# Kernel tuning notes

Hardware: AMD Instinct MI355X
Metric: run time of the kernel (lower is better)

The kernel has to match this reference:

```python
import jax, jax.numpy as jnp
import numpy as np

B, C, H, W = 8, 512, 64, 64
K = 19       # num classes (Cityscapes)
CT = 256     # transform channels


def _proj(x, w, g, b):
    # 1x1 conv (no bias) + folded eval-mode BatchNorm (per-channel scale g, bias b) + ReLU
    # x: [B,Cin,H,W], w: [Cout,Cin]
    y = jnp.einsum('bchw,oc->bohw', x, w)
    return jax.nn.relu(y * g[None, :, None, None] + b[None, :, None, None])


def setup_inputs() -> dict:
    key = jax.random.key(0)
    ks = jax.random.split(key, 12)
    s = lambda i, shape: jax.random.normal(ks[i], shape, jnp.float32) * 0.05
    ones = lambda n: jnp.ones((n,), jnp.float32)
    zeros = lambda n: jnp.zeros((n,), jnp.float32)
    return {
        'x': jax.random.normal(ks[0], (B, C, H, W), jnp.float32),
        'preds': jax.random.normal(ks[1], (B, K, H, W), jnp.float32),
        'feats_il': jax.random.normal(ks[2], (B, C, H, W), jnp.float32),
        # query_project: two 1x1 conv+BN+ReLU blocks
        'q_w1': s(3, (CT, C)), 'q_g1': ones(CT), 'q_b1': zeros(CT),
        'q_w2': s(4, (CT, CT)), 'q_g2': ones(CT), 'q_b2': zeros(CT),
        # key_project: two 1x1 conv+BN+ReLU blocks
        'k_w1': s(5, (CT, C)), 'k_g1': ones(CT), 'k_b1': zeros(CT),
        'k_w2': s(6, (CT, CT)), 'k_g2': ones(CT), 'k_b2': zeros(CT),
        # value_project: one 1x1 conv+BN+ReLU (value_out_norm=True)
        'v_w': s(7, (CT, C)), 'v_g': ones(CT), 'v_b': zeros(CT),
        # out_project: one 1x1 conv+BN+ReLU
        'o_w': s(8, (C, CT)), 'o_g': ones(C), 'o_b': zeros(C),
    }


def reference(x, preds, feats_il, q_w1, q_g1, q_b1, q_w2, q_g2, q_b2,
              k_w1, k_g1, k_b1, k_w2, k_g2, k_b2, v_w, v_g, v_b, o_w, o_g, o_b):
    b, c, h, w = x.shape
    k = preds.shape[1]
    hw = h * w
    feats = x.reshape(b, c, hw).transpose(0, 2, 1)        # [B,HW,C]
    logits = preds.reshape(b, k, hw).transpose(0, 2, 1)   # [B,HW,K]
    argmax = jnp.argmax(logits, axis=-1)                  # [B,HW]
    onehot = jax.nn.one_hot(argmax, k, dtype=x.dtype)     # [B,HW,K]
    NEG = jnp.asarray(-1e9, x.dtype)
    masked = jnp.where(onehot > 0, logits, NEG)
    # per-class softmax over the pixels assigned to that class
    wgt = jax.nn.softmax(masked, axis=1)                  # [B,HW,K]
    cls_feat = jnp.einsum('bpk,bpc->bkc', wgt, feats)     # [B,K,C]
    # scatter class descriptor back to every pixel of that class
    feats_sl = jnp.take_along_axis(cls_feat, argmax[:, :, None], axis=1)  # [B,HW,C]
    feats_sl = feats_sl.transpose(0, 2, 1).reshape(b, c, h, w)
    # SelfAttentionBlock: query from inputs, key/value from feats_sl
    q = _proj(_proj(x, q_w1, q_g1, q_b1), q_w2, q_g2, q_b2)
    kk = _proj(_proj(feats_sl, k_w1, k_g1, k_b1), k_w2, k_g2, k_b2)
    v = _proj(feats_sl, v_w, v_g, v_b)
    ct = q.shape[1]
    qf = q.reshape(b, ct, hw).transpose(0, 2, 1)          # [B,HW,CT]
    kf = kk.reshape(b, ct, hw)                            # [B,CT,HW]
    vf = v.reshape(b, ct, hw).transpose(0, 2, 1)          # [B,HW,CT]
    sim = jnp.einsum('bqc,bck->bqk', qf, kf) * (ct ** -0.5)
    attn = jax.nn.softmax(sim, axis=-1)
    ctx = jnp.einsum('bqk,bkc->bqc', attn, vf)            # [B,HW,CT]
    ctx = ctx.transpose(0, 2, 1).reshape(b, ct, h, w)
    return _proj(ctx, o_w, o_g, o_b)
```

## Files before the change

### kernel.cpp

```cpp
#include <hip/hip_runtime.h>
#include <math.h>

#define HW 4096
#define NB 8
#define NK 19
#define CIN 512
#define CTC 256

typedef __attribute__((ext_vector_type(8))) short short8;
typedef __attribute__((ext_vector_type(4))) float f32x4;

__device__ inline unsigned short f2bf(float x) {
  unsigned u = __float_as_uint(x);
  return (unsigned short)((u + 0x7fffu + ((u >> 16) & 1u)) >> 16);
}
__device__ inline float bf2f(unsigned short h) {
  return __uint_as_float(((unsigned)h) << 16);
}
__device__ inline void gload16(const void* g, void* l) {
  __builtin_amdgcn_global_load_lds(
      (const __attribute__((address_space(1))) void*)g,
      (__attribute__((address_space(3))) void*)l, 16, 0, 0);
}

__global__ __launch_bounds__(256) void wk1a(
    const float* __restrict__ w1, const float* __restrict__ w2,
    const float* __restrict__ wo, unsigned short* __restrict__ wb1,
    unsigned short* __restrict__ wb2, unsigned short* __restrict__ wbo,
    uint4* __restrict__ cls_feat_z, const float* __restrict__ preds,
    float* __restrict__ bestg, int* __restrict__ clsg,
    unsigned int* __restrict__ Mu_part, unsigned int* __restrict__ cnt_part) {
  __shared__ unsigned int Mw[NK];
  __shared__ unsigned int Cw[NK];
  int bx = blockIdx.x;
  int tid = threadIdx.x;
  if (bx < 320) {
    int gid = bx * 256 + tid;
    int i = gid * 4;
    const float* src;
    unsigned short* dst;
    int off;
    if (i < 131072) { src = w1; dst = wb1; off = i; }
    else if (i < 196608) { src = w2; dst = wb2; off = i - 131072; }
    else { src = wo; dst = wbo; off = i - 196608; }
    float4 v = *(const float4*)(src + off);
    dst[off + 0] = f2bf(v.x);
    dst[off + 1] = f2bf(v.y);
    dst[off + 2] = f2bf(v.z);
    dst[off + 3] = f2bf(v.w);
    uint4 z = {0u, 0u, 0u, 0u};
    for (int j = gid; j < 19456; j += 81920) cls_feat_z[j] = z;
  } else {
    int bq = bx - 320;
    int b = bq >> 4, pblk = bq & 15;
    if (tid < NK) { Mw[tid] = 0u; Cw[tid] = 0u; }
    __syncthreads();
    int p = pblk * 256 + tid;
    const float* pb = preds + (size_t)b * NK * HW;
    float best = pb[p];
    int bi = 0;
#pragma unroll
    for (int k = 1; k < NK; ++k) {
      float v = pb[k * HW + p];
      if (v > best) { best = v; bi = k; }
    }
    bestg[b * HW + p] = best;
    clsg[b * HW + p] = bi;
    unsigned fb = __float_as_uint(best);
    unsigned key = (fb & 0x80000000u) ? ~fb : (fb | 0x80000000u);
    atomicMax(&Mw[bi], key);
    atomicAdd(&Cw[bi], 1u);
    __syncthreads();
    if (tid < 32) {
      Mu_part[(b * 16 + pblk) * 32 + tid] = (tid < NK) ? Mw[tid] : 0u;
      cnt_part[(b * 16 + pblk) * 32 + tid] = (tid < NK) ? Cw[tid] : 0u;
    }
  }
}

__global__ __launch_bounds__(256) void k1b(
    float* __restrict__ bestg, const int* __restrict__ clsg,
    const unsigned int* __restrict__ Mu_part, float* __restrict__ Zf_part) {
  int b = blockIdx.y, pblk = blockIdx.x;
  int tid = threadIdx.x;
  __shared__ float Mf[NK];
  __shared__ float Zw[NK];
  if (tid < NK) {
    unsigned key = 0u;
#pragma unroll
    for (int j = 0; j < 16; ++j) {
      unsigned v = Mu_part[(b * 16 + j) * 32 + tid];
      key = (v > key) ? v : key;
    }
    float m = -1e30f;
    if (key) {
      unsigned fb = (key & 0x80000000u) ? (key & 0x7fffffffu) : ~key;
      m = __uint_as_float(fb);
    }
    Mf[tid] = m;
    Zw[tid] = 0.f;
  }
  __syncthreads();
  int p = pblk * 256 + tid;
  int c = clsg[b * HW + p];
  float e = expf(bestg[b * HW + p] - Mf[c]);
  bestg[b * HW + p] = e;
  atomicAdd(&Zw[c], e);
  __syncthreads();
  if (tid < 32) Zf_part[(b * 16 + pblk) * 32 + tid] = (tid < NK) ? Zw[tid] : 0.f;
}

__global__ __launch_bounds__(256) void xk2(
    const float* __restrict__ x, const float* __restrict__ eg,
    const int* __restrict__ clsg, const float* __restrict__ Zf_part,
    unsigned short* __restrict__ xT, float* __restrict__ cls_feat) {
  __shared__ float tile[64][65];
  __shared__ unsigned short Bs[32 * 516];
  __shared__ float Zl[NK];
  int b = blockIdx.z, c0 = blockIdx.y * 64, pbase = blockIdx.x * 512;
  int tid = threadIdx.x;
  int l = tid & 63, w = tid >> 6;
  if (tid < NK) {
    float s = 0.f;
#pragma unroll
    for (int j = 0; j < 16; ++j) s += Zf_part[(b * 16 + j) * 32 + tid];
    Zl[tid] = s;
  }
  {
    uint4 z = {0u, 0u, 0u, 0u};
    for (int i = tid; i < 2064; i += 256) ((uint4*)Bs)[i] = z;
  }
  __syncthreads();
  for (int i = tid; i < 512; i += 256) {
    int c = clsg[b * HW + pbase + i];
    Bs[c * 516 + i] = f2bf(eg[b * HW + pbase + i] / Zl[c]);
  }
  f32x4 acc[2];
  acc[0] = (f32x4){0.f, 0.f, 0.f, 0.f};
  acc[1] = (f32x4){0.f, 0.f, 0.f, 0.f};
  int cbase = w * 16;
  for (int s = 0; s < 8; ++s) {
    int ps = pbase + s * 64;
    __syncthreads();
#pragma unroll
    for (int r = 0; r < 4; ++r) {
      int cl = r * 16 + (tid >> 4);
      int pl = (tid & 15) * 4;
      float4 v = *(const float4*)&x[((size_t)b * CIN + c0 + cl) * HW + ps + pl];
      tile[cl][pl + 0] = v.x;
      tile[cl][pl + 1] = v.y;
      tile[cl][pl + 2] = v.z;
      tile[cl][pl + 3] = v.w;
    }
    __syncthreads();
#pragma unroll
    for (int j = 0; j < 16; ++j) {
      int ploc = j * 4 + w;
      xT[((size_t)b * HW + ps + ploc) * CIN + c0 + l] = f2bf(tile[l][ploc]);
    }
#pragma unroll
    for (int ch = 0; ch < 2; ++ch) {
      int pt = ch * 32 + (l >> 4) * 8;
      union { short8 v; unsigned short u[8]; } af;
      const float* tp = &tile[cbase + (l & 15)][pt];
#pragma unroll
      for (int j = 0; j < 8; ++j) af.u[j] = f2bf(tp[j]);
      int pg = s * 64 + pt;
#pragma unroll
      for (int mf = 0; mf < 2; ++mf) {
        short8 bf = *(const short8*)&Bs[(mf * 16 + (l & 15)) * 516 + pg];
        acc[mf] =
            __builtin_amdgcn_mfma_f32_16x16x32_bf16(af.v, bf, acc[mf], 0, 0, 0);
      }
    }
  }
#pragma unroll
  for (int mf = 0; mf < 2; ++mf) {
    int k = mf * 16 + (l & 15);
    if (k < NK) {
#pragma unroll
      for (int r = 0; r < 4; ++r) {
        int c = c0 + cbase + (l >> 4) * 4 + r;
        atomicAdd(&cls_feat[((size_t)b * NK + k) * CIN + c], acc[mf][r]);
      }
    }
  }
}

__global__ __launch_bounds__(256) void k3a(
    const float* __restrict__ cls_feat, const float* __restrict__ kw1,
    const float* __restrict__ kg1, const float* __restrict__ kb1,
    const float* __restrict__ vw, const float* __restrict__ vg,
    const float* __restrict__ vb, float* __restrict__ h1g,
    float* __restrict__ Vcls) {
  int bk = blockIdx.y;
  int b = bk / NK, kc = bk % NK;
  int q = blockIdx.x;
  __shared__ float cf[CIN];
  int tid = threadIdx.x;
  const float* row = cls_feat + (size_t)bk * CIN;
  for (int i = tid; i < CIN; i += 256) cf[i] = row[i];
  __syncthreads();
  int o = tid >> 1, half = tid & 1;
  int col = q * 64 + (o & 63);
  const float* w =
      (o < 64) ? &kw1[(size_t)col * CIN] : &vw[(size_t)col * CIN];
  int base = half * 256;
  float acc[4] = {0.f, 0.f, 0.f, 0.f};
#pragma unroll 8
  for (int i = 0; i < 64; ++i) {
    float4 w4 = *(const float4*)&w[base + i * 4];
    const float* c4 = &cf[base + i * 4];
    acc[i & 3] += w4.x * c4[0] + w4.y * c4[1] + w4.z * c4[2] + w4.w * c4[3];
  }
  float s = (acc[0] + acc[1]) + (acc[2] + acc[3]);
  s += __shfl_xor(s, 1);
  if (half == 0) {
    if (o < 64) {
      h1g[(size_t)bk * CTC + col] = fmaxf(s * kg1[col] + kb1[col], 0.f);
    } else {
      Vcls[((size_t)b * CTC + col) * NK + kc] =
          fmaxf(s * vg[col] + vb[col], 0.f);
    }
  }
}

__global__ __launch_bounds__(256) void k3b(
    const float* __restrict__ h1g, const float* __restrict__ kw2,
    const float* __restrict__ kg2, const float* __restrict__ kb2,
    unsigned short* __restrict__ KclsT) {
  int bk = blockIdx.y;
  int q = blockIdx.x;
  __shared__ float h1[CTC];
  int tid = threadIdx.x;
  const float* row = h1g + (size_t)bk * CTC;
  if (tid < CTC) h1[tid] = row[tid];
  __syncthreads();
  int o = tid >> 2, part = tid & 3;
  int col = q * 64 + o;
  const float* w = &kw2[(size_t)col * CTC + part * 64];
  const float* c = &h1[part * 64];
  float acc[4] = {0.f, 0.f, 0.f, 0.f};
#pragma unroll
  for (int i = 0; i < 16; ++i) {
    float4 w4 = *(const float4*)&w[i * 4];
    acc[i & 3] += w4.x * c[i * 4] + w4.y * c[i * 4 + 1] + w4.z * c[i * 4 + 2] +
                  w4.w * c[i * 4 + 3];
  }
  float s = (acc[0] + acc[1]) + (acc[2] + acc[3]);
  s += __shfl_xor(s, 1);
  s += __shfl_xor(s, 2);
  if (part == 0)
    KclsT[(size_t)bk * CTC + col] = f2bf(fmaxf(s * kg2[col] + kb2[col], 0.f));
}

__global__ __launch_bounds__(512, 1) void g1g2k5o(
    const unsigned short* __restrict__ xT, const unsigned short* __restrict__ W1,
    const float* __restrict__ g1, const float* __restrict__ b1,
    const unsigned short* __restrict__ W2, const float* __restrict__ g2,
    const float* __restrict__ b2, const unsigned short* __restrict__ KclsT,
    const float* __restrict__ Vcls, const unsigned int* __restrict__ cnt_part,
    const unsigned short* __restrict__ Wo, const float* __restrict__ og,
    const float* __restrict__ ob, float* __restrict__ out) {
  __shared__ __align__(16) char RC[49152];
  __shared__ __align__(16) unsigned short Q1f[8][4096];
  __shared__ __align__(16) unsigned short Kl2[32 * 32 * 8];
  __shared__ __align__(16) unsigned short Vl2[4 * 256 * 8];
  __shared__ float cntl[NK];
  unsigned short* As = (unsigned short*)RC;
  unsigned short* Bs = (unsigned short*)(RC + 16384);
  float* simT = (float*)RC;
  unsigned short* Pl = (unsigned short*)(RC + 16896);
  unsigned short* WoBuf = (unsigned short*)RC;

  int b = blockIdx.y;
  int p0 = blockIdx.x * 128;
  int tid = threadIdx.x;
  int l = tid & 63, w = tid >> 6;
  int wp = w & 3, wm = w >> 2;
  const unsigned short* xTb = xT + ((size_t)b * HW + p0) * CIN;

  for (int i = tid; i < NK * 32; i += 512) {
    int m = i >> 5, s = i & 31;
    short8 v = *(const short8*)&KclsT[((size_t)b * NK + m) * CTC + s * 8];
    *(short8*)&Kl2[(s * 32 + m) * 8] = v;
  }
  for (int i = tid; i < 4 * 256; i += 512) {
    int s = i >> 8, c = i & 255;
    union { short8 v; unsigned short u[8]; } pk;
    const float* vr = &Vcls[((size_t)b * CTC + c) * NK];
#pragma unroll
    for (int j = 0; j < 8; ++j) {
      int k = s * 8 + j;
      pk.u[j] = (k < NK) ? f2bf(vr[k]) : (unsigned short)0;
    }
    *(short8*)&Vl2[(s * 256 + c) * 8] = pk.v;
  }
  if (tid < NK) {
    unsigned int s = 0u;
#pragma unroll
    for (int j = 0; j < 16; ++j) s += cnt_part[(b * 16 + j) * 32 + tid];
    cntl[tid] = (float)s;
  }

  f32x4 acc[2][8];

  auto STAGE_A1 = [&](int buf, int t) {
    int k0 = t * 32;
    int e = tid * 8;
    int rl = e >> 5, sl = (e >> 3) & 3;
    gload16(xTb + (size_t)rl * CIN + k0 + 8 * (sl ^ ((rl >> 1) & 3)),
            &As[buf * 4096 + w * 512]);
  };
  auto STAGE_B1 = [&](int buf, int t) {
    int k0 = t * 32;
#pragma unroll
    for (int q = 0; q < 2; ++q) {
      int e = q * 4096 + tid * 8;
      int rl = e >> 5, sl = (e >> 3) & 3;
      gload16(W1 + (size_t)rl * CIN + k0 + 8 * (sl ^ ((rl >> 1) & 3)),
              &Bs[buf * 8192 + q * 4096 + w * 512]);
    }
  };
#pragma unroll
  for (int i = 0; i < 2; ++i)
#pragma unroll
    for (int j = 0; j < 8; ++j) acc[i][j] = (f32x4){0.f, 0.f, 0.f, 0.f};
  STAGE_A1(0, 0);
  STAGE_B1(0, 0);
  for (int t = 0; t < 16; ++t) {
    __syncthreads();
    if (t + 1 < 16) { STAGE_A1((t + 1) & 1, t + 1); STAGE_B1((t + 1) & 1, t + 1); }
    int cur = t & 1;
    short8 af[2];
#pragma unroll
    for (int f = 0; f < 2; ++f) {
      int nl = wp * 32 + f * 16 + (l & 15);
      af[f] =
          *(const short8*)&As[cur * 4096 + nl * 32 + 8 * ((l >> 4) ^ ((nl >> 1) & 3))];
    }
#pragma unroll
    for (int mf = 0; mf < 8; ++mf) {
      int ml = wm * 128 + mf * 16 + (l & 15);
      short8 bf =
          *(const short8*)&Bs[cur * 8192 + ml * 32 + 8 * ((l >> 4) ^ ((ml >> 1) & 3))];
      acc[0][mf] =
          __builtin_amdgcn_mfma_f32_16x16x32_bf16(af[0], bf, acc[0][mf], 0, 0, 0);
      acc[1][mf] =
          __builtin_amdgcn_mfma_f32_16x16x32_bf16(af[1], bf, acc[1][mf], 0, 0, 0);
    }
  }
#pragma unroll
  for (int mf = 0; mf < 8; ++mf) {
    int ch = wm * 128 + mf * 16 + (l & 15);
    float gm = g1[ch], bm = b1[ch];
    int tq = ch >> 5, slot = (ch >> 3) & 3, wi = ch & 7;
#pragma unroll
    for (int i = 0; i < 2; ++i) {
#pragma unroll
      for (int r = 0; r < 4; ++r) {
        int p = wp * 32 + i * 16 + (l >> 4) * 4 + r;
        Q1f[tq][p * 32 + 8 * (slot ^ ((p >> 1) & 3)) + wi] =
            f2bf(fmaxf(acc[i][mf][r] * gm + bm, 0.f));
      }
    }
  }

  auto STAGE_B2 = [&](int buf, int t) {
    int k0 = t * 32;
#pragma unroll
    for (int q = 0; q < 2; ++q) {
      int e = q * 4096 + tid * 8;
      int rl = e >> 5, sl = (e >> 3) & 3;
      gload16(W2 + (size_t)rl * CTC + k0 + 8 * (sl ^ ((rl >> 1) & 3)),
              &Bs[buf * 8192 + q * 4096 + w * 512]);
    }
  };
#pragma unroll
  for (int i = 0; i < 2; ++i)
#pragma unroll
    for (int j = 0; j < 8; ++j) acc[i][j] = (f32x4){0.f, 0.f, 0.f, 0.f};
  STAGE_B2(0, 0);
  for (int t = 0; t < 8; ++t) {
    __syncthreads();
    if (t + 1 < 8) STAGE_B2((t + 1) & 1, t + 1);
    int cur = t & 1;
    short8 af[2];
#pragma unroll
    for (int f = 0; f < 2; ++f) {
      int nl = wp * 32 + f * 16 + (l & 15);
      af[f] = *(const short8*)&Q1f[t][nl * 32 + 8 * ((l >> 4) ^ ((nl >> 1) & 3))];
    }
#pragma unroll
    for (int mf = 0; mf < 8; ++mf) {
      int ml = wm * 128 + mf * 16 + (l & 15);
      short8 bf =
          *(const short8*)&Bs[cur * 8192 + ml * 32 + 8 * ((l >> 4) ^ ((ml >> 1) & 3))];
      acc[0][mf] =
          __builtin_amdgcn_mfma_f32_16x16x32_bf16(af[0], bf, acc[0][mf], 0, 0, 0);
      acc[1][mf] =
          __builtin_amdgcn_mfma_f32_16x16x32_bf16(af[1], bf, acc[1][mf], 0, 0, 0);
    }
  }
  __syncthreads();
#pragma unroll
  for (int mf = 0; mf < 8; ++mf) {
    int ch = wm * 128 + mf * 16 + (l & 15);
    float gm = g2[ch], bm = b2[ch];
    int tq = ch >> 5, slot = (ch >> 3) & 3, wi = ch & 7;
#pragma unroll
    for (int i = 0; i < 2; ++i) {
#pragma unroll
      for (int r = 0; r < 4; ++r) {
        int p = wp * 32 + i * 16 + (l >> 4) * 4 + r;
        Q1f[tq][p * 32 + 8 * (slot ^ ((p >> 1) & 3)) + wi] =
            f2bf(fmaxf(acc[i][mf][r] * gm + bm, 0.f));
      }
    }
  }
  __syncthreads();

  f32x4 a2[2];
  a2[0] = (f32x4){0.f, 0.f, 0.f, 0.f};
  a2[1] = (f32x4){0.f, 0.f, 0.f, 0.f};
  for (int t = 0; t < 8; ++t) {
    int nl = w * 16 + (l & 15);
    short8 aq =
        *(const short8*)&Q1f[t][nl * 32 + 8 * ((l >> 4) ^ ((nl >> 1) & 3))];
    int s = t * 4 + (l >> 4);
#pragma unroll
    for (int j = 0; j < 2; ++j) {
      int ml = j * 16 + (l & 15);
      short8 bk = *(const short8*)&Kl2[(s * 32 + ml) * 8];
      a2[j] = __builtin_amdgcn_mfma_f32_16x16x32_bf16(aq, bk, a2[j], 0, 0, 0);
    }
  }
  __syncthreads();
#pragma unroll
  for (int j = 0; j < 2; ++j) {
    int m = j * 16 + (l & 15);
    if (m < NK) {
#pragma unroll
      for (int r = 0; r < 4; ++r) {
        int p = w * 16 + (l >> 4) * 4 + r;
        simT[p * 33 + m] = a2[j][r];
      }
    }
  }
  __syncthreads();
  if (tid < 128) {
    float sims[NK];
#pragma unroll
    for (int k = 0; k < NK; ++k) sims[k] = simT[tid * 33 + k] * 0.0625f;
    float m = -1e30f;
#pragma unroll
    for (int k = 0; k < NK; ++k)
      if (cntl[k] > 0.f) m = fmaxf(m, sims[k]);
    float d = 0.f;
#pragma unroll
    for (int k = 0; k < NK; ++k) {
      float e = (cntl[k] > 0.f) ? expf(sims[k] - m) : 0.f;
      sims[k] = cntl[k] * e;
      d += sims[k];
    }
    float inv = 1.f / d;
#pragma unroll
    for (int s = 0; s < 4; ++s) {
      union { short8 v; unsigned short u8[8]; } pk;
#pragma unroll
      for (int j = 0; j < 8; ++j) {
        int k = s * 8 + j;
        pk.u8[j] = (k < NK) ? f2bf(sims[k] * inv) : (unsigned short)0;
      }
      *(short8*)&Pl[(s * 128 + tid) * 8] = pk.v;
    }
  }
  __syncthreads();
  short8 ap;
  {
    int nl = w * 16 + (l & 15);
    ap = *(const short8*)&Pl[((l >> 4) * 128 + nl) * 8];
  }
#pragma unroll
  for (int mc = 0; mc < 4; ++mc) {
#pragma unroll
    for (int mf = 0; mf < 4; ++mf) {
      int ml = mc * 64 + mf * 16 + (l & 15);
      short8 bv = *(const short8*)&Vl2[((l >> 4) * 256 + ml) * 8];
      f32x4 z = {0.f, 0.f, 0.f, 0.f};
      f32x4 o = __builtin_amdgcn_mfma_f32_16x16x32_bf16(ap, bv, z, 0, 0, 0);
      int tq = ml >> 5, slot = (ml >> 3) & 3, wi = ml & 7;
#pragma unroll
      for (int r = 0; r < 4; ++r) {
        int p = w * 16 + (l >> 4) * 4 + r;
        Q1f[tq][p * 32 + 8 * (slot ^ ((p >> 1) & 3)) + wi] = f2bf(o[r]);
      }
    }
  }

  f32x4 a5[2][16];
#pragma unroll
  for (int i = 0; i < 2; ++i)
#pragma unroll
    for (int j = 0; j < 16; ++j) a5[i][j] = (f32x4){0.f, 0.f, 0.f, 0.f};
  for (int t = 0; t < 8; ++t) {
    __syncthreads();
#pragma unroll
    for (int q = 0; q < 4; ++q) {
      int e = q * 4096 + tid * 8;
      int rl = e >> 5, sl = (e >> 3) & 3;
      gload16(Wo + (size_t)rl * CTC + t * 32 + 8 * (sl ^ ((rl >> 1) & 3)),
              &WoBuf[q * 4096 + w * 512]);
    }
    __syncthreads();
    short8 af[2];
#pragma unroll
    for (int f = 0; f < 2; ++f) {
      int nl = wp * 32 + f * 16 + (l & 15);
      af[f] = *(const short8*)&Q1f[t][nl * 32 + 8 * ((l >> 4) ^ ((nl >> 1) & 3))];
    }
#pragma unroll
    for (int mf = 0; mf < 16; ++mf) {
      int ml = wm * 256 + mf * 16 + (l & 15);
      short8 bf =
          *(const short8*)&WoBuf[ml * 32 + 8 * ((l >> 4) ^ ((ml >> 1) & 3))];
      a5[0][mf] =
          __builtin_amdgcn_mfma_f32_16x16x32_bf16(af[0], bf, a5[0][mf], 0, 0, 0);
      a5[1][mf] =
          __builtin_amdgcn_mfma_f32_16x16x32_bf16(af[1], bf, a5[1][mf], 0, 0, 0);
    }
  }
  float* outb = out + (size_t)b * CIN * HW;
#pragma unroll
  for (int mf = 0; mf < 16; ++mf) {
    int co = wm * 256 + mf * 16 + (l & 15);
    float gm = og[co], bm = ob[co];
#pragma unroll
    for (int i = 0; i < 2; ++i) {
      int n = p0 + wp * 32 + i * 16 + (l >> 4) * 4;
      float4 o;
      o.x = fmaxf(a5[i][mf][0] * gm + bm, 0.f);
      o.y = fmaxf(a5[i][mf][1] * gm + bm, 0.f);
      o.z = fmaxf(a5[i][mf][2] * gm + bm, 0.f);
      o.w = fmaxf(a5[i][mf][3] * gm + bm, 0.f);
      *(float4*)&outb[(size_t)co * HW + n] = o;
    }
  }
}

extern "C" void kernel_launch(void* const* d_in, const int* in_sizes, int n_in,
                              void* d_out, int out_size, void* d_ws, size_t ws_size,
                              hipStream_t stream) {
  const float* x = (const float*)d_in[0];
  const float* preds = (const float*)d_in[1];
  const float* q_w1 = (const float*)d_in[3];
  const float* q_g1 = (const float*)d_in[4];
  const float* q_b1 = (const float*)d_in[5];
  const float* q_w2 = (const float*)d_in[6];
  const float* q_g2 = (const float*)d_in[7];
  const float* q_b2 = (const float*)d_in[8];
  const float* k_w1 = (const float*)d_in[9];
  const float* k_g1 = (const float*)d_in[10];
  const float* k_b1 = (const float*)d_in[11];
  const float* k_w2 = (const float*)d_in[12];
  const float* k_g2 = (const float*)d_in[13];
  const float* k_b2 = (const float*)d_in[14];
  const float* v_w = (const float*)d_in[15];
  const float* v_g = (const float*)d_in[16];
  const float* v_b = (const float*)d_in[17];
  const float* o_w = (const float*)d_in[18];
  const float* o_g = (const float*)d_in[19];
  const float* o_b = (const float*)d_in[20];
  float* out = (float*)d_out;

  char* base = (char*)d_ws;
  unsigned short* xT = (unsigned short*)base;
  char* f32r = base + 33554432;
  float* cls_feat = (float*)f32r;
  unsigned short* KclsT = (unsigned short*)(f32r + 311296);
  float* Vcls = (float*)(f32r + 389120);
  unsigned short* wb1 = (unsigned short*)(f32r + 544768);
  unsigned short* wb2 = (unsigned short*)(f32r + 806912);
  unsigned short* wbo = (unsigned short*)(f32r + 937984);
  float* h1g = (float*)(f32r + 1200128);
  float* bestg = (float*)(f32r + 1355776);
  int* clsg = (int*)(f32r + 1486848);
  unsigned int* Mu_part = (unsigned int*)(f32r + 1617920);
  unsigned int* cnt_part = (unsigned int*)(f32r + 1634304);
  float* Zf_part = (float*)(f32r + 1650688);

  wk1a<<<448, 256, 0, stream>>>(q_w1, q_w2, o_w, wb1, wb2, wbo,
                                (uint4*)cls_feat, preds, bestg, clsg, Mu_part,
                                cnt_part);
  k1b<<<dim3(16, NB), 256, 0, stream>>>(bestg, clsg, Mu_part, Zf_part);
  xk2<<<dim3(8, 8, NB), 256, 0, stream>>>(x, bestg, clsg, Zf_part, xT,
                                          cls_feat);
  k3a<<<dim3(4, NB * NK), 256, 0, stream>>>(cls_feat, k_w1, k_g1, k_b1, v_w,
                                            v_g, v_b, h1g, Vcls);
  k3b<<<dim3(4, NB * NK), 256, 0, stream>>>(h1g, k_w2, k_g2, k_b2, KclsT);
  g1g2k5o<<<dim3(HW / 128, NB), 512, 0, stream>>>(xT, wb1, q_g1, q_b1, wb2,
                                                  q_g2, q_b2, KclsT, Vcls,
                                                  cnt_part, wbo, o_g, o_b,
                                                  out);
}
```

Measured before the change: 113.3 us.

## Halve fused kernel tile to 64 pixels with 256 threads and two blocks per CU

The fused query/attention/output kernel now handles 64 pixels per block with 256 threads instead of 128 pixels with 512, which doubles the grid to 512 blocks and targets two resident blocks per CU through launch bounds and aliased shared memory. The K/V class tables are loaded later, into reused scratch space, and the output projection is split into two 256-channel halves with a double-buffered weight pipeline. This shrinks the accumulator register footprint. In exchange, each block re-reads every weight matrix for half as many pixels, so total weight traffic roughly doubles.

New measurement: 115.8 us. 1.02x slower.

```diff
diff --git a/kernel.cpp b/kernel.cpp
--- a/kernel.cpp
+++ b/kernel.cpp
@@ -254,7 +254,7 @@
     KclsT[(size_t)bk * CTC + col] = f2bf(fmaxf(s * kg2[col] + kb2[col], 0.f));
 }
 
-__global__ __launch_bounds__(512, 1) void g1g2k5o(
+__global__ __launch_bounds__(256, 2) void g1g2k5o(
     const unsigned short* __restrict__ xT, const unsigned short* __restrict__ W1,
     const float* __restrict__ g1, const float* __restrict__ b1,
     const unsigned short* __restrict__ W2, const float* __restrict__ g2,
@@ -262,40 +262,25 @@
     const float* __restrict__ Vcls, const unsigned int* __restrict__ cnt_part,
     const unsigned short* __restrict__ Wo, const float* __restrict__ og,
     const float* __restrict__ ob, float* __restrict__ out) {
-  __shared__ __align__(16) char RC[49152];
-  __shared__ __align__(16) unsigned short Q1f[8][4096];
-  __shared__ __align__(16) unsigned short Kl2[32 * 32 * 8];
-  __shared__ __align__(16) unsigned short Vl2[4 * 256 * 8];
+  __shared__ __align__(16) char SMQ[32768];
+  __shared__ __align__(16) char SMR[45568];
   __shared__ float cntl[NK];
-  unsigned short* As = (unsigned short*)RC;
-  unsigned short* Bs = (unsigned short*)(RC + 16384);
-  float* simT = (float*)RC;
-  unsigned short* Pl = (unsigned short*)(RC + 16896);
-  unsigned short* WoBuf = (unsigned short*)RC;
+  unsigned short* Q1f = (unsigned short*)SMQ;
+  unsigned short* As = (unsigned short*)SMR;
+  unsigned short* Bs = (unsigned short*)(SMR + 8192);
+  unsigned short* Kl2 = (unsigned short*)SMR;
+  unsigned short* Vl2 = (unsigned short*)(SMR + 16384);
+  float* simT = (float*)(SMR + 32768);
+  unsigned short* Pl = (unsigned short*)(SMR + 41216);
+  unsigned short* WoBuf = (unsigned short*)SMR;
 
   int b = blockIdx.y;
-  int p0 = blockIdx.x * 128;
+  int p0 = blockIdx.x * 64;
   int tid = threadIdx.x;
   int l = tid & 63, w = tid >> 6;
-  int wp = w & 3, wm = w >> 2;
+  int wp = w & 1, wm = w >> 1;
   const unsigned short* xTb = xT + ((size_t)b * HW + p0) * CIN;
 
-  for (int i = tid; i < NK * 32; i += 512) {
-    int m = i >> 5, s = i & 31;
-    short8 v = *(const short8*)&KclsT[((size_t)b * NK + m) * CTC + s * 8];
-    *(short8*)&Kl2[(s * 32 + m) * 8] = v;
-  }
-  for (int i = tid; i < 4 * 256; i += 512) {
-    int s = i >> 8, c = i & 255;
-    union { short8 v; unsigned short u[8]; } pk;
-    const float* vr = &Vcls[((size_t)b * CTC + c) * NK];
-#pragma unroll
-    for (int j = 0; j < 8; ++j) {
-      int k = s * 8 + j;
-      pk.u[j] = (k < NK) ? f2bf(vr[k]) : (unsigned short)0;
-    }
-    *(short8*)&Vl2[(s * 256 + c) * 8] = pk.v;
-  }
   if (tid < NK) {
     unsigned int s = 0u;
 #pragma unroll
@@ -310,16 +295,16 @@
     int e = tid * 8;
     int rl = e >> 5, sl = (e >> 3) & 3;
     gload16(xTb + (size_t)rl * CIN + k0 + 8 * (sl ^ ((rl >> 1) & 3)),
-            &As[buf * 4096 + w * 512]);
+            &As[buf * 2048 + w * 512]);
   };
   auto STAGE_B1 = [&](int buf, int t) {
     int k0 = t * 32;
 #pragma unroll
-    for (int q = 0; q < 2; ++q) {
-      int e = q * 4096 + tid * 8;
+    for (int q = 0; q < 4; ++q) {
+      int e = q * 2048 + tid * 8;
       int rl = e >> 5, sl = (e >> 3) & 3;
       gload16(W1 + (size_t)rl * CIN + k0 + 8 * (sl ^ ((rl >> 1) & 3)),
-              &Bs[buf * 8192 + q * 4096 + w * 512]);
+              &Bs[buf * 8192 + q * 2048 + w * 512]);
     }
   };
 #pragma unroll
@@ -337,7 +322,7 @@
     for (int f = 0; f < 2; ++f) {
       int nl = wp * 32 + f * 16 + (l & 15);
       af[f] =
-          *(const short8*)&As[cur * 4096 + nl * 32 + 8 * ((l >> 4) ^ ((nl >> 1) & 3))];
+          *(const short8*)&As[cur * 2048 + nl * 32 + 8 * ((l >> 4) ^ ((nl >> 1) & 3))];
     }
 #pragma unroll
     for (int mf = 0; mf < 8; ++mf) {
@@ -360,7 +345,7 @@
 #pragma unroll
       for (int r = 0; r < 4; ++r) {
         int p = wp * 32 + i * 16 + (l >> 4) * 4 + r;
-        Q1f[tq][p * 32 + 8 * (slot ^ ((p >> 1) & 3)) + wi] =
+        Q1f[tq * 2048 + p * 32 + 8 * (slot ^ ((p >> 1) & 3)) + wi] =
             f2bf(fmaxf(acc[i][mf][r] * gm + bm, 0.f));
       }
     }
@@ -369,11 +354,11 @@
   auto STAGE_B2 = [&](int buf, int t) {
     int k0 = t * 32;
 #pragma unroll
-    for (int q = 0; q < 2; ++q) {
-      int e = q * 4096 + tid * 8;
+    for (int q = 0; q < 4; ++q) {
+      int e = q * 2048 + tid * 8;
       int rl = e >> 5, sl = (e >> 3) & 3;
       gload16(W2 + (size_t)rl * CTC + k0 + 8 * (sl ^ ((rl >> 1) & 3)),
-              &Bs[buf * 8192 + q * 4096 + w * 512]);
+              &Bs[buf * 8192 + q * 2048 + w * 512]);
     }
   };
 #pragma unroll
@@ -389,7 +374,8 @@
 #pragma unroll
     for (int f = 0; f < 2; ++f) {
       int nl = wp * 32 + f * 16 + (l & 15);
-      af[f] = *(const short8*)&Q1f[t][nl * 32 + 8 * ((l >> 4) ^ ((nl >> 1) & 3))];
+      af[f] =
+          *(const short8*)&Q1f[t * 2048 + nl * 32 + 8 * ((l >> 4) ^ ((nl >> 1) & 3))];
     }
 #pragma unroll
     for (int mf = 0; mf < 8; ++mf) {
@@ -413,10 +399,26 @@
 #pragma unroll
       for (int r = 0; r < 4; ++r) {
         int p = wp * 32 + i * 16 + (l >> 4) * 4 + r;
-        Q1f[tq][p * 32 + 8 * (slot ^ ((p >> 1) & 3)) + wi] =
+        Q1f[tq * 2048 + p * 32 + 8 * (slot ^ ((p >> 1) & 3)) + wi] =
             f2bf(fmaxf(acc[i][mf][r] * gm + bm, 0.f));
       }
     }
+  }
+  for (int i = tid; i < NK * 32; i += 256) {
+    int m = i >> 5, s = i & 31;
+    short8 v = *(const short8*)&KclsT[((size_t)b * NK + m) * CTC + s * 8];
+    *(short8*)&Kl2[(s * 32 + m) * 8] = v;
+  }
+  for (int i = tid; i < 4 * 256; i += 256) {
+    int s = i >> 8, c = i & 255;
+    union { short8 v; unsigned short u[8]; } pk;
+    const float* vr = &Vcls[((size_t)b * CTC + c) * NK];
+#pragma unroll
+    for (int j = 0; j < 8; ++j) {
+      int k = s * 8 + j;
+      pk.u[j] = (k < NK) ? f2bf(vr[k]) : (unsigned short)0;
+    }
+    *(short8*)&Vl2[(s * 256 + c) * 8] = pk.v;
   }
   __syncthreads();
 
@@ -426,7 +428,7 @@
   for (int t = 0; t < 8; ++t) {
     int nl = w * 16 + (l & 15);
     short8 aq =
-        *(const short8*)&Q1f[t][nl * 32 + 8 * ((l >> 4) ^ ((nl >> 1) & 3))];
+        *(const short8*)&Q1f[t * 2048 + nl * 32 + 8 * ((l >> 4) ^ ((nl >> 1) & 3))];
     int s = t * 4 + (l >> 4);
 #pragma unroll
     for (int j = 0; j < 2; ++j) {
@@ -448,7 +450,7 @@
     }
   }
   __syncthreads();
-  if (tid < 128) {
+  if (tid < 64) {
     float sims[NK];
 #pragma unroll
     for (int k = 0; k < NK; ++k) sims[k] = simT[tid * 33 + k] * 0.0625f;
@@ -472,14 +474,14 @@
         int k = s * 8 + j;
         pk.u8[j] = (k < NK) ? f2bf(sims[k] * inv) : (unsigned short)0;
       }
-      *(short8*)&Pl[(s * 128 + tid) * 8] = pk.v;
+      *(short8*)&Pl[(s * 64 + tid) * 8] = pk.v;
     }
   }
   __syncthreads();
   short8 ap;
   {
     int nl = w * 16 + (l & 15);
-    ap = *(const short8*)&Pl[((l >> 4) * 128 + nl) * 8];
+    ap = *(const short8*)&Pl[((l >> 4) * 64 + nl) * 8];
   }
 #pragma unroll
   for (int mc = 0; mc < 4; ++mc) {
@@ -493,57 +495,65 @@
 #pragma unroll
       for (int r = 0; r < 4; ++r) {
         int p = w * 16 + (l >> 4) * 4 + r;
-        Q1f[tq][p * 32 + 8 * (slot ^ ((p >> 1) & 3)) + wi] = f2bf(o[r]);
-      }
-    }
-  }
-
-  f32x4 a5[2][16];
-#pragma unroll
-  for (int i = 0; i < 2; ++i)
-#pragma unroll
-    for (int j = 0; j < 16; ++j) a5[i][j] = (f32x4){0.f, 0.f, 0.f, 0.f};
-  for (int t = 0; t < 8; ++t) {
-    __syncthreads();
+        Q1f[tq * 2048 + p * 32 + 8 * (slot ^ ((p >> 1) & 3)) + wi] = f2bf(o[r]);
+      }
+    }
+  }
+
+  auto STAGE_WO = [&](int hm, int buf, int t) {
+    int k0 = t * 32;
 #pragma unroll
     for (int q = 0; q < 4; ++q) {
-      int e = q * 4096 + tid * 8;
+      int e = q * 2048 + tid * 8;
       int rl = e >> 5, sl = (e >> 3) & 3;
-      gload16(Wo + (size_t)rl * CTC + t * 32 + 8 * (sl ^ ((rl >> 1) & 3)),
-              &WoBuf[q * 4096 + w * 512]);
-    }
-    __syncthreads();
-    short8 af[2];
-#pragma unroll
-    for (int f = 0; f < 2; ++f) {
-      int nl = wp * 32 + f * 16 + (l & 15);
-      af[f] = *(const short8*)&Q1f[t][nl * 32 + 8 * ((l >> 4) ^ ((nl >> 1) & 3))];
-    }
-#pragma unroll
-    for (int mf = 0; mf < 16; ++mf) {
-      int ml = wm * 256 + mf * 16 + (l & 15);
-      short8 bf =
-          *(const short8*)&WoBuf[ml * 32 + 8 * ((l >> 4) ^ ((ml >> 1) & 3))];
-      a5[0][mf] =
-          __builtin_amdgcn_mfma_f32_16x16x32_bf16(af[0], bf, a5[0][mf], 0, 0, 0);
-      a5[1][mf] =
-          __builtin_amdgcn_mfma_f32_16x16x32_bf16(af[1], bf, a5[1][mf], 0, 0, 0);
-    }
-  }
+      gload16(Wo + (size_t)(hm * 256 + rl) * CTC + k0 + 8 * (sl ^ ((rl >> 1) & 3)),
+              &WoBuf[buf * 8192 + q * 2048 + w * 512]);
+    }
+  };
   float* outb = out + (size_t)b * CIN * HW;
-#pragma unroll
-  for (int mf = 0; mf < 16; ++mf) {
-    int co = wm * 256 + mf * 16 + (l & 15);
-    float gm = og[co], bm = ob[co];
-#pragma unroll
-    for (int i = 0; i < 2; ++i) {
-      int n = p0 + wp * 32 + i * 16 + (l >> 4) * 4;
-      float4 o;
-      o.x = fmaxf(a5[i][mf][0] * gm + bm, 0.f);
-      o.y = fmaxf(a5[i][mf][1] * gm + bm, 0.f);
-      o.z = fmaxf(a5[i][mf][2] * gm + bm, 0.f);
-      o.w = fmaxf(a5[i][mf][3] * gm + bm, 0.f);
-      *(float4*)&outb[(size_t)co * HW + n] = o;
+  STAGE_WO(0, 0, 0);
+  for (int hm = 0; hm < 2; ++hm) {
+#pragma unroll
+    for (int i = 0; i < 2; ++i)
+#pragma unroll
+      for (int j = 0; j < 8; ++j) acc[i][j] = (f32x4){0.f, 0.f, 0.f, 0.f};
+    for (int t = 0; t < 8; ++t) {
+      __syncthreads();
+      if (t + 1 < 8) STAGE_WO(hm, (t + 1) & 1, t + 1);
+      int cur = t & 1;
+      short8 af[2];
+#pragma unroll
+      for (int f = 0; f < 2; ++f) {
+        int nl = wp * 32 + f * 16 + (l & 15);
+        af[f] =
+            *(const short8*)&Q1f[t * 2048 + nl * 32 + 8 * ((l >> 4) ^ ((nl >> 1) & 3))];
+      }
+#pragma unroll
+      for (int mf = 0; mf < 8; ++mf) {
+        int ml = wm * 128 + mf * 16 + (l & 15);
+        short8 bf =
+            *(const short8*)&WoBuf[cur * 8192 + ml * 32 + 8 * ((l >> 4) ^ ((ml >> 1) & 3))];
+        acc[0][mf] =
+            __builtin_amdgcn_mfma_f32_16x16x32_bf16(af[0], bf, acc[0][mf], 0, 0, 0);
+        acc[1][mf] =
+            __builtin_amdgcn_mfma_f32_16x16x32_bf16(af[1], bf, acc[1][mf], 0, 0, 0);
+      }
+    }
+    if (hm == 0) STAGE_WO(1, 0, 0);
+#pragma unroll
+    for (int mf = 0; mf < 8; ++mf) {
+      int co = hm * 256 + wm * 128 + mf * 16 + (l & 15);
+      float gm = og[co], bm = ob[co];
+#pragma unroll
+      for (int i = 0; i < 2; ++i) {
+        int n = p0 + wp * 32 + i * 16 + (l >> 4) * 4;
+        float4 o;
+        o.x = fmaxf(acc[i][mf][0] * gm + bm, 0.f);
+        o.y = fmaxf(acc[i][mf][1] * gm + bm, 0.f);
+        o.z = fmaxf(acc[i][mf][2] * gm + bm, 0.f);
+        o.w = fmaxf(acc[i][mf][3] * gm + bm, 0.f);
+        *(float4*)&outb[(size_t)co * HW + n] = o;
+      }
     }
   }
 }
@@ -598,8 +608,8 @@
   k3a<<<dim3(4, NB * NK), 256, 0, stream>>>(cls_feat, k_w1, k_g1, k_b1, v_w,
                                             v_g, v_b, h1g, Vcls);
   k3b<<<dim3(4, NB * NK), 256, 0, stream>>>(h1g, k_w2, k_g2, k_b2, KclsT);
-  g1g2k5o<<<dim3(HW / 128, NB), 512, 0, stream>>>(xT, wb1, q_g1, q_b1, wb2,
-                                                  q_g2, q_b2, KclsT, Vcls,
-                                                  cnt_part, wbo, o_g, o_b,
-                                                  out);
-}
+  g1g2k5o<<<dim3(HW / 64, NB), 256, 0, stream>>>(xT, wb1, q_g1, q_b1, wb2,
+                                                 q_g2, q_b2, KclsT, Vcls,
+                                                 cnt_part, wbo, o_g, o_b,
+                                                 out);
+}
```
